# Performance work log

Hardware: AMD Instinct MI355X
Metric: run time of the kernel (lower is better)

Reference implementation:

```python
import jax, jax.numpy as jnp
import numpy as np

B, S, MW = 128, 256, 21          # batch, sentence length, max word length
VOCAB, E_CHAR, E_WORD, K = 100, 50, 256, 5


def setup_inputs() -> dict:
    key = jax.random.key(0)
    ks = jax.random.split(key, 6)
    padded_sents = jax.random.randint(ks[0], (B, S, MW), 0, VOCAB)
    emb_table = jax.random.normal(ks[1], (VOCAB, E_CHAR), jnp.float32) * 0.1
    emb_table = emb_table.at[0].set(0.0)  # pad_token_idx row zeroed (padding_idx)
    conv_w = jax.random.normal(ks[2], (E_WORD, E_CHAR, K), jnp.float32) * 0.05
    conv_b = jnp.zeros((E_WORD,), jnp.float32)
    w_proj = jax.random.normal(ks[3], (E_WORD, E_WORD), jnp.float32) * 0.05
    b_proj = jnp.zeros((E_WORD,), jnp.float32)
    w_gate = jax.random.normal(ks[4], (E_WORD, E_WORD), jnp.float32) * 0.05
    b_gate = jnp.zeros((E_WORD,), jnp.float32)
    return {
        "padded_sents": padded_sents,
        "emb_table": emb_table,
        "conv_w": conv_w,
        "conv_b": conv_b,
        "w_proj": w_proj,
        "b_proj": b_proj,
        "w_gate": w_gate,
        "b_gate": b_gate,
    }


def reference(padded_sents, emb_table, conv_w, conv_b, w_proj, b_proj, w_gate, b_gate):
    b, s, mw = padded_sents.shape
    # char embedding lookup: [B,S,MW,E_CHAR]
    x = emb_table[padded_sents]
    # fold (B,S) into one batch dim and move channels first: [B*S, E_CHAR, MW]
    x = x.reshape(b * s, mw, -1).transpose(0, 2, 1)
    # Conv1d VALID over char positions: [B*S, E_WORD, MW-K+1]
    y = jax.lax.conv_general_dilated(
        x, conv_w, window_strides=(1,), padding="VALID",
        dimension_numbers=("NCH", "OIH", "NCH"))
    y = jax.nn.relu(y + conv_b[None, :, None])
    # max-pool over remaining char positions: [B*S, E_WORD]
    y = jnp.max(y, axis=2)
    # Highway network
    proj = jax.nn.relu(y @ w_proj.T + b_proj)
    gate = jax.nn.sigmoid(y @ w_gate.T + b_gate)
    out = gate * proj + (1.0 - gate) * y
    # dropout in eval mode (identity)
    return out.reshape(b, s, -1)
```

## Files before the change

### kernel.cpp

```cpp
#include <hip/hip_runtime.h>

#define B_     128
#define S_     256
#define MW_    21
#define VOCAB_ 100
#define EC_    50
#define EW_    256
#define KW_    5
#define T_     17
#define NW_    (B_ * S_)
#define GROWS  (VOCAB_ * KW_)
#define WPB    128

typedef _Float16 f16x8 __attribute__((ext_vector_type(8)));
typedef float    f32x4 __attribute__((ext_vector_type(4)));

__global__ __launch_bounds__(256) void k_prep(const float* __restrict__ emb,
                                              const float* __restrict__ cw,
                                              const float* __restrict__ Wp,
                                              const float* __restrict__ Wg,
                                              _Float16* __restrict__ g,
                                              _Float16* __restrict__ wpf,
                                              _Float16* __restrict__ wgf) {
  const int bi = blockIdx.x;
  if (bi < GROWS) {
    __shared__ float es[EC_];
    const int v = bi / KW_;
    const int k = bi % KW_;
    const int o = threadIdx.x;
    if (threadIdx.x < EC_) es[threadIdx.x] = emb[v * EC_ + threadIdx.x];
    __syncthreads();
    float acc = 0.f;
#pragma unroll
    for (int i = 0; i < EC_; ++i)
      acc += es[i] * cw[(o * EC_ + i) * KW_ + k];
    g[bi * EW_ + o] = (_Float16)acc;
  } else {
    const int fl  = (bi - GROWS) * 256 + threadIdx.x;
    const int nt  = fl >> 9;
    const int rem = fl & 511;
    const int ks  = rem >> 6;
    const int l   = rem & 63;
    const int n   = nt * 16 + (l & 15);
    const int kc  = ks * 32 + (l >> 4) * 8;
    const int src = n * EW_ + kc;
    const float4 p0 = *(const float4*)&Wp[src], p1 = *(const float4*)&Wp[src + 4];
    const float4 q0 = *(const float4*)&Wg[src], q1 = *(const float4*)&Wg[src + 4];
    f16x8 hp = {(_Float16)p0.x, (_Float16)p0.y, (_Float16)p0.z, (_Float16)p0.w,
                (_Float16)p1.x, (_Float16)p1.y, (_Float16)p1.z, (_Float16)p1.w};
    f16x8 hg = {(_Float16)q0.x, (_Float16)q0.y, (_Float16)q0.z, (_Float16)q0.w,
                (_Float16)q1.x, (_Float16)q1.y, (_Float16)q1.z, (_Float16)q1.w};
    *(f16x8*)&wpf[fl * 8] = hp;
    *(f16x8*)&wgf[fl * 8] = hg;
  }
}

__global__ __launch_bounds__(512, 2) void k_mega(const int* __restrict__ idx,
                                                 const _Float16* __restrict__ g,
                                                 const float* __restrict__ cb,
                                                 const _Float16* __restrict__ wpf,
                                                 const _Float16* __restrict__ wgf,
                                                 const float* __restrict__ bp,
                                                 const float* __restrict__ bg,
                                                 float* __restrict__ out) {
  __shared__ __align__(16) _Float16 lds[32768 + GROWS * 64];
  _Float16* y_s = lds;
  _Float16* g_s = lds + 32768;

  const int tid  = threadIdx.x;
  const int wave = tid >> 6, lane = tid & 63;
  const int m0 = blockIdx.x * WPB;

  const int wq = lane >> 3, og = lane & 7;
#pragma unroll
  for (int chunk = 0; chunk < 4; ++chunk) {
    const int oc0 = chunk * 64;
    for (int c = tid; c < GROWS * 8; c += 512) {
      const int row = c >> 3, cc = c & 7;
      const int v = (row * 205) >> 10;
      *(f16x8*)&g_s[row * 64 + ((cc ^ (v & 7)) * 8)] =
          *(const f16x8*)&g[row * EW_ + oc0 + cc * 8];
    }
    __syncthreads();

    f16x8 bias;
#pragma unroll
    for (int j = 0; j < 8; ++j) bias[j] = (_Float16)cb[oc0 + og * 8 + j];

    const int ks_w    = chunk * 2 + (og >> 2);
    const int lane_hi = (og & 3) << 4;

#pragma unroll
    for (int it = 0; it < 2; ++it) {
      const int wl = it * 64 + wave * 8 + wq;
      const int* __restrict__ ip = idx + (m0 + wl) * MW_;
      int base[MW_];
#pragma unroll
      for (int c = 0; c < MW_; ++c) {
        const int v = ip[c];
        base[c] = v * (KW_ * 64) + ((og ^ (v & 7)) * 8);
      }

      const _Float16 NEG = (_Float16)(-60000.0f);
      f16x8 mx = {NEG, NEG, NEG, NEG, NEG, NEG, NEG, NEG};
#pragma unroll
      for (int t = 0; t < T_; ++t) {
        f16x8 s = *(const f16x8*)&g_s[base[t]];
#pragma unroll
        for (int k = 1; k < KW_; ++k)
          s += *(const f16x8*)&g_s[base[t + k] + k * 64];
        mx = __builtin_elementwise_max(mx, s);
      }
      const f16x8 zero8 = {0, 0, 0, 0, 0, 0, 0, 0};
      mx = __builtin_elementwise_max(mx + bias, zero8);

      const int mt = wl >> 4;
      const int lane_t = (wl & 15) | lane_hi;
      *(f16x8*)&y_s[((mt * 8 + ks_w) * 64 + lane_t) * 8] = mx;
    }
    __syncthreads();
  }

  const int mtp = wave >> 1, nh = wave & 1;
  const int quad = lane >> 4, r16 = lane & 15;

  f16x8 a[2][8];
#pragma unroll
  for (int mi = 0; mi < 2; ++mi)
#pragma unroll
    for (int ks = 0; ks < 8; ++ks)
      a[mi][ks] = *(const f16x8*)&y_s[(((mtp * 2 + mi) * 8 + ks) * 64 + lane) * 8];

  const f32x4 zero = {0.f, 0.f, 0.f, 0.f};
#pragma unroll
  for (int h = 0; h < 2; ++h) {
    f32x4 accp[2][4], accg[2][4];
#pragma unroll
    for (int mi = 0; mi < 2; ++mi)
#pragma unroll
      for (int nf = 0; nf < 4; ++nf) { accp[mi][nf] = zero; accg[mi][nf] = zero; }

#pragma unroll
    for (int nf = 0; nf < 4; ++nf) {
      const int nt = h * 8 + nh * 4 + nf;
#pragma unroll
      for (int ks = 0; ks < 8; ++ks) {
        const int off = ((nt * 8 + ks) * 64 + lane) * 8;
        const f16x8 bpv = *(const f16x8*)&wpf[off];
        const f16x8 bgv = *(const f16x8*)&wgf[off];
#pragma unroll
        for (int mi = 0; mi < 2; ++mi) {
          accp[mi][nf] = __builtin_amdgcn_mfma_f32_16x16x32_f16(a[mi][ks], bpv, accp[mi][nf], 0, 0, 0);
          accg[mi][nf] = __builtin_amdgcn_mfma_f32_16x16x32_f16(a[mi][ks], bgv, accg[mi][nf], 0, 0, 0);
        }
      }
    }

#pragma unroll
    for (int mi = 0; mi < 2; ++mi) {
      const int mt = mtp * 2 + mi;
#pragma unroll
      for (int nf = 0; nf < 4; ++nf) {
        const int n = h * 128 + nh * 64 + nf * 16 + r16;
        const float bpn = bp[n];
        const float bgn = bg[n];
        const int ks_e = n >> 5;
        const int lane_e = ((n >> 3) & 3) << 4;
        const int je = n & 7;
#pragma unroll
        for (int reg = 0; reg < 4; ++reg) {
          const int m = mt * 16 + quad * 4 + reg;
          float p = fmaxf(accp[mi][nf][reg] + bpn, 0.f);
          const float gz = accg[mi][nf][reg] + bgn;
          const float gate = 1.f / (1.f + __expf(-gz));
          const float yv = (float)y_s[((mt * 8 + ks_e) * 64 + ((m & 15) | lane_e)) * 8 + je];
          out[(m0 + m) * EW_ + n] = gate * p + (1.f - gate) * yv;
        }
      }
    }
  }
}

extern "C" void kernel_launch(void* const* d_in, const int* in_sizes, int n_in,
                              void* d_out, int out_size, void* d_ws, size_t ws_size,
                              hipStream_t stream) {
  (void)in_sizes; (void)n_in; (void)out_size; (void)ws_size;
  const int*   idx = (const int*)d_in[0];
  const float* emb = (const float*)d_in[1];
  const float* cw  = (const float*)d_in[2];
  const float* cb  = (const float*)d_in[3];
  const float* wp  = (const float*)d_in[4];
  const float* bpp = (const float*)d_in[5];
  const float* wgt = (const float*)d_in[6];
  const float* bgg = (const float*)d_in[7];
  float* out = (float*)d_out;
  _Float16* g_ws = (_Float16*)d_ws;
  _Float16* wp_f = g_ws + GROWS * EW_;
  _Float16* wg_f = wp_f + EW_ * EW_;

  k_prep<<<GROWS + 32, 256, 0, stream>>>(emb, cw, wp, wgt, g_ws, wp_f, wg_f);
  k_mega<<<NW_ / WPB, 512, 0, stream>>>(idx, g_ws, cb, wp_f, wg_f, bpp, bgg, out);
}
```

Before: 130.7 us.

## Shrink fused conv-highway block to 32 words with 256 threads, drop LDS swizzle

Cuts words per block from 128 to 32 and threads from 512 to 256. Each wave now handles one word per chunk and one M-tile across a full N half in the highway GEMM. The XOR swizzle on the staged conv table is removed, simplifying addressing. The intent is more, smaller blocks for better CU coverage. The cost is that every block restages the full 64KB-per-chunk conv table, so table and weight traffic per word rises, and bank conflicts in the gather may return.

```diff
diff --git a/kernel.cpp b/kernel.cpp
--- a/kernel.cpp
+++ b/kernel.cpp
@@ -10,7 +10,7 @@
 #define T_     17
 #define NW_    (B_ * S_)
 #define GROWS  (VOCAB_ * KW_)
-#define WPB    128
+#define WPB    32
 
 typedef _Float16 f16x8 __attribute__((ext_vector_type(8)));
 typedef float    f32x4 __attribute__((ext_vector_type(4)));
@@ -55,7 +55,7 @@
   }
 }
 
-__global__ __launch_bounds__(512, 2) void k_mega(const int* __restrict__ idx,
+__global__ __launch_bounds__(256, 2) void k_mega(const int* __restrict__ idx,
                                                  const _Float16* __restrict__ g,
                                                  const float* __restrict__ cb,
                                                  const _Float16* __restrict__ wpf,
@@ -63,9 +63,9 @@
                                                  const float* __restrict__ bp,
                                                  const float* __restrict__ bg,
                                                  float* __restrict__ out) {
-  __shared__ __align__(16) _Float16 lds[32768 + GROWS * 64];
+  __shared__ __align__(16) _Float16 lds[8192 + GROWS * 64];
   _Float16* y_s = lds;
-  _Float16* g_s = lds + 32768;
+  _Float16* g_s = lds + 8192;
 
   const int tid  = threadIdx.x;
   const int wave = tid >> 6, lane = tid & 63;
@@ -75,11 +75,9 @@
 #pragma unroll
   for (int chunk = 0; chunk < 4; ++chunk) {
     const int oc0 = chunk * 64;
-    for (int c = tid; c < GROWS * 8; c += 512) {
+    for (int c = tid; c < GROWS * 8; c += 256) {
       const int row = c >> 3, cc = c & 7;
-      const int v = (row * 205) >> 10;
-      *(f16x8*)&g_s[row * 64 + ((cc ^ (v & 7)) * 8)] =
-          *(const f16x8*)&g[row * EW_ + oc0 + cc * 8];
+      *(f16x8*)&g_s[row * 64 + cc * 8] = *(const f16x8*)&g[row * EW_ + oc0 + cc * 8];
     }
     __syncthreads();
 
@@ -90,93 +88,74 @@
     const int ks_w    = chunk * 2 + (og >> 2);
     const int lane_hi = (og & 3) << 4;
 
+    const int wl = wave * 8 + wq;
+    const int* __restrict__ ip = idx + (m0 + wl) * MW_;
+    int base[MW_];
 #pragma unroll
-    for (int it = 0; it < 2; ++it) {
-      const int wl = it * 64 + wave * 8 + wq;
-      const int* __restrict__ ip = idx + (m0 + wl) * MW_;
-      int base[MW_];
+    for (int c = 0; c < MW_; ++c)
+      base[c] = ip[c] * (KW_ * 64) + og * 8;
+
+    const _Float16 NEG = (_Float16)(-60000.0f);
+    f16x8 mx = {NEG, NEG, NEG, NEG, NEG, NEG, NEG, NEG};
 #pragma unroll
-      for (int c = 0; c < MW_; ++c) {
-        const int v = ip[c];
-        base[c] = v * (KW_ * 64) + ((og ^ (v & 7)) * 8);
-      }
+    for (int t = 0; t < T_; ++t) {
+      f16x8 s = *(const f16x8*)&g_s[base[t]];
+#pragma unroll
+      for (int k = 1; k < KW_; ++k)
+        s += *(const f16x8*)&g_s[base[t + k] + k * 64];
+      mx = __builtin_elementwise_max(mx, s);
+    }
+    const f16x8 zero8 = {0, 0, 0, 0, 0, 0, 0, 0};
+    mx = __builtin_elementwise_max(mx + bias, zero8);
 
-      const _Float16 NEG = (_Float16)(-60000.0f);
-      f16x8 mx = {NEG, NEG, NEG, NEG, NEG, NEG, NEG, NEG};
-#pragma unroll
-      for (int t = 0; t < T_; ++t) {
-        f16x8 s = *(const f16x8*)&g_s[base[t]];
-#pragma unroll
-        for (int k = 1; k < KW_; ++k)
-          s += *(const f16x8*)&g_s[base[t + k] + k * 64];
-        mx = __builtin_elementwise_max(mx, s);
-      }
-      const f16x8 zero8 = {0, 0, 0, 0, 0, 0, 0, 0};
-      mx = __builtin_elementwise_max(mx + bias, zero8);
-
-      const int mt = wl >> 4;
-      const int lane_t = (wl & 15) | lane_hi;
-      *(f16x8*)&y_s[((mt * 8 + ks_w) * 64 + lane_t) * 8] = mx;
-    }
+    const int mt = wl >> 4;
+    const int lane_t = (wl & 15) | lane_hi;
+    *(f16x8*)&y_s[((mt * 8 + ks_w) * 64 + lane_t) * 8] = mx;
     __syncthreads();
   }
 
-  const int mtp = wave >> 1, nh = wave & 1;
+  const int mt = wave >> 1, nh = wave & 1;
   const int quad = lane >> 4, r16 = lane & 15;
 
-  f16x8 a[2][8];
+  f16x8 a[8];
 #pragma unroll
-  for (int mi = 0; mi < 2; ++mi)
-#pragma unroll
-    for (int ks = 0; ks < 8; ++ks)
-      a[mi][ks] = *(const f16x8*)&y_s[(((mtp * 2 + mi) * 8 + ks) * 64 + lane) * 8];
+  for (int ks = 0; ks < 8; ++ks)
+    a[ks] = *(const f16x8*)&y_s[((mt * 8 + ks) * 64 + lane) * 8];
 
   const f32x4 zero = {0.f, 0.f, 0.f, 0.f};
+  f32x4 accp[8], accg[8];
 #pragma unroll
-  for (int h = 0; h < 2; ++h) {
-    f32x4 accp[2][4], accg[2][4];
-#pragma unroll
-    for (int mi = 0; mi < 2; ++mi)
-#pragma unroll
-      for (int nf = 0; nf < 4; ++nf) { accp[mi][nf] = zero; accg[mi][nf] = zero; }
+  for (int nf = 0; nf < 8; ++nf) { accp[nf] = zero; accg[nf] = zero; }
 
 #pragma unroll
-    for (int nf = 0; nf < 4; ++nf) {
-      const int nt = h * 8 + nh * 4 + nf;
+  for (int nf = 0; nf < 8; ++nf) {
+    const int nt = nh * 8 + nf;
 #pragma unroll
-      for (int ks = 0; ks < 8; ++ks) {
-        const int off = ((nt * 8 + ks) * 64 + lane) * 8;
-        const f16x8 bpv = *(const f16x8*)&wpf[off];
-        const f16x8 bgv = *(const f16x8*)&wgf[off];
-#pragma unroll
-        for (int mi = 0; mi < 2; ++mi) {
-          accp[mi][nf] = __builtin_amdgcn_mfma_f32_16x16x32_f16(a[mi][ks], bpv, accp[mi][nf], 0, 0, 0);
-          accg[mi][nf] = __builtin_amdgcn_mfma_f32_16x16x32_f16(a[mi][ks], bgv, accg[mi][nf], 0, 0, 0);
-        }
-      }
+    for (int ks = 0; ks < 8; ++ks) {
+      const int off = ((nt * 8 + ks) * 64 + lane) * 8;
+      const f16x8 bpv = *(const f16x8*)&wpf[off];
+      const f16x8 bgv = *(const f16x8*)&wgf[off];
+      accp[nf] = __builtin_amdgcn_mfma_f32_16x16x32_f16(a[ks], bpv, accp[nf], 0, 0, 0);
+      accg[nf] = __builtin_amdgcn_mfma_f32_16x16x32_f16(a[ks], bgv, accg[nf], 0, 0, 0);
     }
+  }
 
 #pragma unroll
-    for (int mi = 0; mi < 2; ++mi) {
-      const int mt = mtp * 2 + mi;
+  for (int nf = 0; nf < 8; ++nf) {
+    const int n = nh * 128 + nf * 16 + r16;
+    const float bpn = bp[n];
+    const float bgn = bg[n];
+    const int ks_e = n >> 5;
+    const int lane_e = ((n >> 3) & 3) << 4;
+    const int je = n & 7;
 #pragma unroll
-      for (int nf = 0; nf < 4; ++nf) {
-        const int n = h * 128 + nh * 64 + nf * 16 + r16;
-        const float bpn = bp[n];
-        const float bgn = bg[n];
-        const int ks_e = n >> 5;
-        const int lane_e = ((n >> 3) & 3) << 4;
-        const int je = n & 7;
-#pragma unroll
-        for (int reg = 0; reg < 4; ++reg) {
-          const int m = mt * 16 + quad * 4 + reg;
-          float p = fmaxf(accp[mi][nf][reg] + bpn, 0.f);
-          const float gz = accg[mi][nf][reg] + bgn;
-          const float gate = 1.f / (1.f + __expf(-gz));
-          const float yv = (float)y_s[((mt * 8 + ks_e) * 64 + ((m & 15) | lane_e)) * 8 + je];
-          out[(m0 + m) * EW_ + n] = gate * p + (1.f - gate) * yv;
-        }
-      }
+    for (int reg = 0; reg < 4; ++reg) {
+      const int m = mt * 16 + quad * 4 + reg;
+      float p = fmaxf(accp[nf][reg] + bpn, 0.f);
+      const float gz = accg[nf][reg] + bgn;
+      const float gate = 1.f / (1.f + __expf(-gz));
+      const float yv = (float)y_s[((mt * 8 + ks_e) * 64 + ((m & 15) | lane_e)) * 8 + je];
+      out[(m0 + m) * EW_ + n] = gate * p + (1.f - gate) * yv;
     }
   }
 }
@@ -199,5 +178,5 @@
   _Float16* wg_f = wp_f + EW_ * EW_;
 
   k_prep<<<GROWS + 32, 256, 0, stream>>>(emb, cw, wp, wgt, g_ws, wp_f, wg_f);
-  k_mega<<<NW_ / WPB, 512, 0, stream>>>(idx, g_ws, cb, wp_f, wg_f, bpp, bgg, out);
+  k_mega<<<NW_ / WPB, 256, 0, stream>>>(idx, g_ws, cb, wp_f, wg_f, bpp, bgg, out);
 }
```

Result: slower. 154.7 us (+18.3%).

## Prefetch next g chunk into registers and move LDS swizzle from g_s to y_s

Applied to the files above, without the earlier changes.

Each 64-channel slice of the gather table is now loaded from global memory into registers while the current chunk's conv/max work runs, then stored to LDS after a barrier. This hides global-load latency behind compute and removes one barrier per chunk from the critical path. The XOR swizzle on g_s is dropped, so gather reads index g_s linearly. A new XOR swizzle is applied to the y_s store, the MFMA A-fragment loads and the epilogue reads. The prefetch holds eight f16x8 registers per thread, and the unswizzled g_s reads may cause more LDS bank conflicts.

```diff
diff --git a/kernel.cpp b/kernel.cpp
--- a/kernel.cpp
+++ b/kernel.cpp
@@ -70,18 +70,32 @@
   const int tid  = threadIdx.x;
   const int wave = tid >> 6, lane = tid & 63;
   const int m0 = blockIdx.x * WPB;
-
   const int wq = lane >> 3, og = lane & 7;
+
+#pragma unroll
+  for (int i = 0; i < 8; ++i) {
+    const int c = tid + i * 512;
+    if (c < GROWS * 8) {
+      const int row = c >> 3, cc = c & 7;
+      *(f16x8*)&g_s[row * 64 + cc * 8] = *(const f16x8*)&g[row * EW_ + cc * 8];
+    }
+  }
+  __syncthreads();
+
+  f16x8 pre[8];
 #pragma unroll
   for (int chunk = 0; chunk < 4; ++chunk) {
     const int oc0 = chunk * 64;
-    for (int c = tid; c < GROWS * 8; c += 512) {
-      const int row = c >> 3, cc = c & 7;
-      const int v = (row * 205) >> 10;
-      *(f16x8*)&g_s[row * 64 + ((cc ^ (v & 7)) * 8)] =
-          *(const f16x8*)&g[row * EW_ + oc0 + cc * 8];
-    }
-    __syncthreads();
+    if (chunk < 3) {
+#pragma unroll
+      for (int i = 0; i < 8; ++i) {
+        const int c = tid + i * 512;
+        if (c < GROWS * 8) {
+          const int row = c >> 3, cc = c & 7;
+          pre[i] = *(const f16x8*)&g[row * EW_ + oc0 + 64 + cc * 8];
+        }
+      }
+    }
 
     f16x8 bias;
 #pragma unroll
@@ -96,10 +110,8 @@
       const int* __restrict__ ip = idx + (m0 + wl) * MW_;
       int base[MW_];
 #pragma unroll
-      for (int c = 0; c < MW_; ++c) {
-        const int v = ip[c];
-        base[c] = v * (KW_ * 64) + ((og ^ (v & 7)) * 8);
-      }
+      for (int c = 0; c < MW_; ++c)
+        base[c] = ip[c] * (KW_ * 64) + og * 8;
 
       const _Float16 NEG = (_Float16)(-60000.0f);
       f16x8 mx = {NEG, NEG, NEG, NEG, NEG, NEG, NEG, NEG};
@@ -115,10 +127,21 @@
       mx = __builtin_elementwise_max(mx + bias, zero8);
 
       const int mt = wl >> 4;
-      const int lane_t = (wl & 15) | lane_hi;
-      *(f16x8*)&y_s[((mt * 8 + ks_w) * 64 + lane_t) * 8] = mx;
+      const int lt = ((wl & 15) | lane_hi) ^ og;
+      *(f16x8*)&y_s[((mt * 8 + ks_w) * 64 + lt) * 8] = mx;
     }
     __syncthreads();
+    if (chunk < 3) {
+#pragma unroll
+      for (int i = 0; i < 8; ++i) {
+        const int c = tid + i * 512;
+        if (c < GROWS * 8) {
+          const int row = c >> 3, cc = c & 7;
+          *(f16x8*)&g_s[row * 64 + cc * 8] = pre[i];
+        }
+      }
+      __syncthreads();
+    }
   }
 
   const int mtp = wave >> 1, nh = wave & 1;
@@ -128,8 +151,10 @@
 #pragma unroll
   for (int mi = 0; mi < 2; ++mi)
 #pragma unroll
-    for (int ks = 0; ks < 8; ++ks)
-      a[mi][ks] = *(const f16x8*)&y_s[(((mtp * 2 + mi) * 8 + ks) * 64 + lane) * 8];
+    for (int ks = 0; ks < 8; ++ks) {
+      const int key = ((ks & 1) << 2) | quad;
+      a[mi][ks] = *(const f16x8*)&y_s[(((mtp * 2 + mi) * 8 + ks) * 64 + (lane ^ key)) * 8];
+    }
 
   const f32x4 zero = {0.f, 0.f, 0.f, 0.f};
 #pragma unroll
@@ -166,6 +191,7 @@
         const float bgn = bg[n];
         const int ks_e = n >> 5;
         const int lane_e = ((n >> 3) & 3) << 4;
+        const int og_e = (n >> 3) & 7;
         const int je = n & 7;
 #pragma unroll
         for (int reg = 0; reg < 4; ++reg) {
@@ -173,7 +199,8 @@
           float p = fmaxf(accp[mi][nf][reg] + bpn, 0.f);
           const float gz = accg[mi][nf][reg] + bgn;
           const float gate = 1.f / (1.f + __expf(-gz));
-          const float yv = (float)y_s[((mt * 8 + ks_e) * 64 + ((m & 15) | lane_e)) * 8 + je];
+          const float yv =
+              (float)y_s[((mt * 8 + ks_e) * 64 + (((m & 15) | lane_e) ^ og_e)) * 8 + je];
           out[(m0 + m) * EW_ + n] = gate * p + (1.f - gate) * yv;
         }
       }
```

Result: faster. 125.3 us (-4.2%).
